# Kernel optimization log

Hardware: AMD Instinct MI355X
Metric: run time of the kernel (lower is better)

Reference implementation:

```python
import jax, jax.numpy as jnp
import numpy as np

D = 64          # d_model
H = 128         # ffn_hidden_dim
N = 10000       # nodes
E = 50000       # edges
NEG_SLOPE = 0.01  # LeakyReLU default


def setup_inputs() -> dict:
    key = jax.random.key(0)
    ks = jax.random.split(key, 10)
    x = jax.random.normal(ks[0], (N, D), dtype=jnp.float32)
    edge_index = jax.random.randint(ks[1], (2, E), 0, N)
    edge_attr = jax.random.normal(ks[2], (E, D), dtype=jnp.float32)
    # MapE2NxN params (stored as [in, out] so forward is x @ W + b)
    w1 = jax.random.normal(ks[3], (D, H), dtype=jnp.float32) / np.sqrt(D)
    b1 = jnp.zeros((H,), dtype=jnp.float32)
    w2 = jax.random.normal(ks[4], (H, D * D), dtype=jnp.float32) / np.sqrt(H)
    b2 = jnp.zeros((D * D,), dtype=jnp.float32)
    # NNConv root weight + bias
    root = jax.random.normal(ks[5], (D, D), dtype=jnp.float32) / np.sqrt(D)
    bias = jnp.zeros((D,), dtype=jnp.float32)
    # LayerNorm affine params
    gamma = jnp.ones((D,), dtype=jnp.float32)
    beta = jnp.zeros((D,), dtype=jnp.float32)
    return {"x": x, "edge_attr": edge_attr, "gamma": gamma, "beta": beta,
            "w1": w1, "b1": b1, "w2": w2, "b2": b2,
            "root": root, "bias": bias, "edge_index": edge_index}


def _layer_norm(h, gamma, beta, eps=1e-5):
    mu = jnp.mean(h, axis=-1, keepdims=True)
    var = jnp.var(h, axis=-1, keepdims=True)
    return (h - mu) * jax.lax.rsqrt(var + eps) * gamma + beta


def _leaky_relu(h):
    return jnp.where(h >= 0, h, NEG_SLOPE * h)


def reference(x, edge_attr, gamma, beta, w1, b1, w2, b2, root, bias, edge_index):
    src, dst = edge_index[0], edge_index[1]
    # DeepGCNLayer block='res+': pre-activation norm -> act -> (dropout p=0) -> conv -> residual
    h = _leaky_relu(_layer_norm(x, gamma, beta))
    # MapE2NxN on edge attributes -> per-edge [D, D] weight matrix
    we = _leaky_relu(edge_attr @ w1 + b1) @ w2 + b2   # [E, D*D]
    we = we.reshape(E, D, D)
    # per-edge matvec with source node features (PyG NNConv message)
    msg = jnp.einsum('ed,edf->ef', h[src], we)        # [E, D]
    # scatter-mean aggregate into destination nodes
    agg = jax.ops.segment_sum(msg, dst, num_segments=N)
    cnt = jax.ops.segment_sum(jnp.ones((E,), dtype=msg.dtype), dst, num_segments=N)
    agg = agg / jnp.maximum(cnt, 1.0)[:, None]
    # root transform + bias, then residual
    out = agg + h @ root + bias
    return x + out
```

## Files before the change

### kernel.cpp

```cpp
#include <hip/hip_runtime.h>

#define NS 10000
#define DD 64
#define HH 128
#define EE 50000
#define SLOPE 0.01f

typedef __attribute__((ext_vector_type(8))) short short8;
typedef __attribute__((ext_vector_type(4))) float f32x4;

static __device__ __forceinline__ unsigned short f2bf(float f) {
  unsigned int u = __float_as_uint(f);
  u += 0x7fff + ((u >> 16) & 1);
  return (unsigned short)(u >> 16);
}

__device__ __forceinline__ float wave_sum64(float v) {
  #pragma unroll
  for (int m = 32; m >= 1; m >>= 1) v += __shfl_xor(v, m, 64);
  return v;
}

__global__ __launch_bounds__(256) void k_prep(const float* __restrict__ x,
    const float* __restrict__ gamma, const float* __restrict__ beta,
    float* __restrict__ h, unsigned short* __restrict__ hbf,
    const float* __restrict__ ea, unsigned short* __restrict__ eabf,
    const float* __restrict__ w2, unsigned short* __restrict__ w2t2,
    const float* __restrict__ w1, unsigned short* __restrict__ w1t,
    const float* __restrict__ b2, unsigned short* __restrict__ b2t,
    const int* __restrict__ ei, int* __restrict__ cntsrc,
    int* __restrict__ cntdst) {
  int gid = blockIdx.x * 256 + threadIdx.x;
  if (gid < EE) {
    atomicAdd(&cntsrc[ei[gid]], 1);
    atomicAdd(&cntdst[ei[EE + gid]], 1);
  }
  if (gid < EE * DD / 8) {
    const float4* sp = (const float4*)(ea + (size_t)gid * 8);
    float4 v0 = sp[0], v1 = sp[1];
    short8 o;
    o[0] = f2bf(v0.x); o[1] = f2bf(v0.y); o[2] = f2bf(v0.z); o[3] = f2bf(v0.w);
    o[4] = f2bf(v1.x); o[5] = f2bf(v1.y); o[6] = f2bf(v1.z); o[7] = f2bf(v1.w);
    *(short8*)(eabf + (size_t)gid * 8) = o;
  }
  if (gid < HH * DD * DD) {
    int d = gid & 63;
    int c2 = gid >> 6;
    int f = c2 >> 7, k = c2 & 127;
    w2t2[gid] = f2bf(w2[k * (DD * DD) + d * DD + f]);
  }
  if (gid < DD * HH) {
    int d = gid & 63, hc = gid >> 6;
    w1t[gid] = f2bf(w1[d * HH + hc]);
  }
  if (gid < DD * DD) {
    int d = gid & 63, f = gid >> 6;
    b2t[gid] = f2bf(b2[d * DD + f]);
  }
  int wid = threadIdx.x >> 6;
  int lane = threadIdx.x & 63;
  int row = blockIdx.x * 4 + wid;
  if (row >= NS) return;
  float v = x[row * DD + lane];
  float s = wave_sum64(v);
  float s2 = wave_sum64(v * v);
  float mu = s * (1.0f / 64.0f);
  float var = s2 * (1.0f / 64.0f) - mu * mu;
  float r = rsqrtf(var + 1e-5f);
  float hn = (v - mu) * r * gamma[lane] + beta[lane];
  float hv = hn >= 0.f ? hn : SLOPE * hn;
  h[row * DD + lane] = hv;
  hbf[row * DD + lane] = f2bf(hv);
}

__global__ __launch_bounds__(1024) void k_scan(const int* __restrict__ cntsrc,
    int* __restrict__ rowptr, int* __restrict__ cursor) {
  __shared__ int ps[1024];
  int t = threadIdx.x;
  const int CH = (NS + 1023) / 1024;
  int base = t * CH;
  int sum = 0;
  for (int i = 0; i < CH; ++i) {
    int idx = base + i;
    if (idx < NS) sum += cntsrc[idx];
  }
  ps[t] = sum;
  __syncthreads();
  for (int off = 1; off < 1024; off <<= 1) {
    int v = (t >= off) ? ps[t - off] : 0;
    __syncthreads();
    ps[t] += v;
    __syncthreads();
  }
  int run = ps[t] - sum;
  for (int i = 0; i < CH; ++i) {
    int idx = base + i;
    if (idx < NS) {
      rowptr[idx] = run;
      cursor[idx] = run;
      run += cntsrc[idx];
    }
  }
  if (t == 1023) rowptr[NS] = run;
}

#define UBLK 782
#define CBLK 157
__global__ __launch_bounds__(256) void k_mid(
    const unsigned short* __restrict__ eabf, const unsigned short* __restrict__ w1t,
    const float* __restrict__ b1, unsigned short* __restrict__ ubf,
    const unsigned short* __restrict__ hbf, const unsigned short* __restrict__ b2t,
    float* __restrict__ cc, const int* __restrict__ ei,
    int* __restrict__ cursor, int* __restrict__ eord) {
  int t = threadIdx.x;
  int bid = blockIdx.x;
  int gid = bid * 256 + t;
  if (gid < EE) {
    int s = ei[gid];
    int pos = atomicAdd(&cursor[s], 1);
    eord[pos] = gid;
  }
  int w = t >> 6, lane = t & 63, lr = lane & 15, lg = lane >> 4;
  if (bid < UBLK) {
    int r0 = bid * 64 + w * 16;
    int ra = r0 + lr; if (ra >= EE) ra = EE - 1;
    short8 a0 = *(const short8*)(eabf + (size_t)ra * DD + lg * 8);
    short8 a1 = *(const short8*)(eabf + (size_t)ra * DD + 32 + lg * 8);
    short8 bb0[8], bb1[8];
    #pragma unroll
    for (int ni = 0; ni < 8; ++ni) {
      const unsigned short* bp = w1t + (ni * 16 + lr) * DD;
      bb0[ni] = *(const short8*)(bp + lg * 8);
      bb1[ni] = *(const short8*)(bp + 32 + lg * 8);
    }
    f32x4 acc[8] = {};
    #pragma unroll
    for (int ni = 0; ni < 8; ++ni) {
      acc[ni] = __builtin_amdgcn_mfma_f32_16x16x32_bf16(a0, bb0[ni], acc[ni], 0, 0, 0);
      acc[ni] = __builtin_amdgcn_mfma_f32_16x16x32_bf16(a1, bb1[ni], acc[ni], 0, 0, 0);
    }
    #pragma unroll
    for (int ni = 0; ni < 8; ++ni) {
      int col = ni * 16 + lr;
      float bb = b1[col];
      #pragma unroll
      for (int reg = 0; reg < 4; ++reg) {
        int gr = r0 + lg * 4 + reg;
        if (gr < EE) {
          float vv = acc[ni][reg] + bb;
          ubf[(size_t)gr * HH + col] = f2bf(vv >= 0.f ? vv : SLOPE * vv);
        }
      }
    }
  } else if (bid < UBLK + CBLK) {
    int row0 = (bid - UBLK) * 64;
    short8 a[4][2];
    #pragma unroll
    for (int mi = 0; mi < 4; ++mi) {
      int ra = row0 + mi * 16 + lr; if (ra >= NS) ra = NS - 1;
      a[mi][0] = *(const short8*)(hbf + (size_t)ra * DD + lg * 8);
      a[mi][1] = *(const short8*)(hbf + (size_t)ra * DD + 32 + lg * 8);
    }
    const unsigned short* bp = b2t + (w * 16 + lr) * DD;
    short8 b0 = *(const short8*)(bp + lg * 8);
    short8 b1v = *(const short8*)(bp + 32 + lg * 8);
    f32x4 acc[4] = {};
    #pragma unroll
    for (int mi = 0; mi < 4; ++mi) {
      acc[mi] = __builtin_amdgcn_mfma_f32_16x16x32_bf16(a[mi][0], b0, acc[mi], 0, 0, 0);
      acc[mi] = __builtin_amdgcn_mfma_f32_16x16x32_bf16(a[mi][1], b1v, acc[mi], 0, 0, 0);
    }
    #pragma unroll
    for (int mi = 0; mi < 4; ++mi)
      #pragma unroll
      for (int reg = 0; reg < 4; ++reg) {
        int gr = row0 + mi * 16 + lg * 4 + reg;
        if (gr < NS) cc[(size_t)gr * DD + w * 16 + lr] = acc[mi][reg];
      }
  }
}

__global__ __launch_bounds__(256) void k_T_mfma(
    const unsigned short* __restrict__ hbf, const unsigned short* __restrict__ w2t2,
    unsigned short* __restrict__ T, int n0, int n1) {
  __shared__ unsigned short As[64][72];
  __shared__ unsigned short Bs[256 * 72];
  int t = threadIdx.x;
  int row0 = n0 + blockIdx.x * 64;
  int col0 = blockIdx.y * 256;
  #pragma unroll
  for (int i = 0; i < 2; ++i) {
    int idx = t + i * 256;
    int r = idx >> 3, cc = (idx & 7) * 8;
    int gr = row0 + r;
    short8 v = {};
    if (gr < n1) v = *(const short8*)(hbf + (size_t)gr * DD + cc);
    *(short8*)(&As[r][cc]) = v;
  }
  #pragma unroll
  for (int i = 0; i < 8; ++i) {
    int idx = t + i * 256;
    int cL = idx >> 3, rr = (idx & 7) * 8;
    int gc = col0 + cL;
    short8 v = *(const short8*)(w2t2 + (size_t)gc * DD + rr);
    *(short8*)(&Bs[cL * 72 + rr]) = v;
  }
  __syncthreads();
  int w = t >> 6, lane = t & 63;
  int lr = lane & 15, lg = lane >> 4;
  f32x4 acc[4][4] = {};
  #pragma unroll
  for (int kk = 0; kk < 64; kk += 32) {
    short8 a[4], b[4];
    #pragma unroll
    for (int mi = 0; mi < 4; ++mi)
      a[mi] = *(const short8*)(&As[mi * 16 + lr][kk + lg * 8]);
    #pragma unroll
    for (int ni = 0; ni < 4; ++ni)
      b[ni] = *(const short8*)(&Bs[(w * 64 + ni * 16 + lr) * 72 + kk + lg * 8]);
    #pragma unroll
    for (int mi = 0; mi < 4; ++mi)
      #pragma unroll
      for (int ni = 0; ni < 4; ++ni)
        acc[mi][ni] = __builtin_amdgcn_mfma_f32_16x16x32_bf16(
            a[mi], b[ni], acc[mi][ni], 0, 0, 0);
  }
  __syncthreads();
  #pragma unroll
  for (int mi = 0; mi < 4; ++mi)
    #pragma unroll
    for (int ni = 0; ni < 4; ++ni) {
      int col = w * 64 + ni * 16 + lr;
      #pragma unroll
      for (int reg = 0; reg < 4; ++reg)
        Bs[(mi * 16 + lg * 4 + reg) * 268 + col] = f2bf(acc[mi][ni][reg]);
    }
  __syncthreads();
  #pragma unroll
  for (int i = 0; i < 8; ++i) {
    int idx = t + i * 256;
    int row = idx >> 5, seg = idx & 31;
    int gr = row0 + row;
    if (gr < n1) {
      short8 v = *(const short8*)(&Bs[row * 268 + seg * 8]);
      *(short8*)(T + (size_t)(gr - n0) * (HH * DD) + col0 + seg * 8) = v;
    }
  }
}

__global__ __launch_bounds__(256) void k_msg_wave(
    const unsigned short* __restrict__ ubf, const unsigned short* __restrict__ T,
    const float* __restrict__ cc, const int* __restrict__ ei,
    const int* __restrict__ rowptr, const int* __restrict__ eord,
    float* __restrict__ agg, int n0, int n1) {
  int wid = threadIdx.x >> 6;
  int lane = threadIdx.x & 63;
  int s = n0 + blockIdx.x * 4 + wid;
  if (s >= n1) return;
  int beg = rowptr[s];
  int deg = rowptr[s + 1] - beg;
  if (deg == 0) return;
  int lr = lane & 15, lg = lane >> 4;
  int ev = 0, dv = 0;
  if (lane < 16 && lane < deg) {
    ev = eord[beg + lane];
    dv = ei[EE + ev];
  }
  const unsigned short* tp = T + (size_t)(s - n0) * (HH * DD);
  short8 b[4][4];
  #pragma unroll
  for (int ft = 0; ft < 4; ++ft)
    #pragma unroll
    for (int kk = 0; kk < 4; ++kk)
      b[ft][kk] =
          *(const short8*)(tp + (ft * 16 + lr) * HH + kk * 32 + lg * 8);
  float clv[4];
  #pragma unroll
  for (int ft = 0; ft < 4; ++ft) clv[ft] = cc[(size_t)s * DD + ft * 16 + lr];

  for (int p0 = 0; p0 < deg; p0 += 16) {
    if (p0) {
      ev = 0; dv = 0;
      if (lane < 16 && p0 + lane < deg) {
        ev = eord[beg + p0 + lane];
        dv = ei[EE + ev];
      }
    }
    int el = __shfl(ev, (p0 + lr < deg) ? lr : 0);
    const unsigned short* up = ubf + (size_t)el * HH;
    short8 au[4];
    #pragma unroll
    for (int kk = 0; kk < 4; ++kk)
      au[kk] = *(const short8*)(up + kk * 32 + lg * 8);
    f32x4 acc[4] = {};
    #pragma unroll
    for (int kk = 0; kk < 4; ++kk)
      #pragma unroll
      for (int ft = 0; ft < 4; ++ft)
        acc[ft] = __builtin_amdgcn_mfma_f32_16x16x32_bf16(au[kk], b[ft][kk],
                                                          acc[ft], 0, 0, 0);
    #pragma unroll
    for (int reg = 0; reg < 4; ++reg) {
      int eidx = p0 + lg * 4 + reg;
      int dstn = __shfl(dv, lg * 4 + reg);
      if (eidx < deg) {
        #pragma unroll
        for (int ft = 0; ft < 4; ++ft)
          atomicAdd(&agg[(size_t)dstn * DD + ft * 16 + lr],
                    acc[ft][reg] + clv[ft]);
      }
    }
  }
}

__global__ __launch_bounds__(256) void k_final(const float* __restrict__ x,
    const float* __restrict__ h, const float* __restrict__ root,
    const float* __restrict__ bias, const float* __restrict__ agg,
    const int* __restrict__ cnt, float* __restrict__ out) {
  __shared__ float Bs[DD][DD + 1];
  __shared__ float As[32][DD];
  int t = threadIdx.x;
  #pragma unroll
  for (int i = 0; i < 16; ++i) {
    int idx = t + i * 256;
    Bs[idx >> 6][idx & 63] = root[idx];
  }
  int row0 = blockIdx.x * 32;
  #pragma unroll
  for (int i = 0; i < 8; ++i) {
    int idx = t + i * 256;
    int r = idx >> 6, d = idx & 63;
    int gr = row0 + r;
    As[r][d] = (gr < NS) ? h[gr * DD + d] : 0.f;
  }
  __syncthreads();
  int r = t >> 3;
  int c0 = (t & 7) * 8;
  int gr = row0 + r;
  if (gr >= NS) return;
  float acc[8] = {};
  for (int d = 0; d < DD; ++d) {
    float a = As[r][d];
    #pragma unroll
    for (int j = 0; j < 8; ++j) acc[j] += a * Bs[d][c0 + j];
  }
  float inv = 1.0f / fmaxf((float)cnt[gr], 1.0f);
  #pragma unroll
  for (int j = 0; j < 8; ++j) {
    size_t gi = (size_t)gr * DD + c0 + j;
    out[gi] = x[gi] + agg[gi] * inv + acc[j] + bias[c0 + j];
  }
}

extern "C" void kernel_launch(void* const* d_in, const int* in_sizes, int n_in,
                              void* d_out, int out_size, void* d_ws, size_t ws_size,
                              hipStream_t stream) {
  const float* x     = (const float*)d_in[0];
  const float* ea    = (const float*)d_in[1];
  const float* gamma = (const float*)d_in[2];
  const float* beta  = (const float*)d_in[3];
  const float* w1    = (const float*)d_in[4];
  const float* b1    = (const float*)d_in[5];
  const float* w2    = (const float*)d_in[6];
  const float* b2    = (const float*)d_in[7];
  const float* root  = (const float*)d_in[8];
  const float* bias  = (const float*)d_in[9];
  const int*   ei    = (const int*)d_in[10];
  float* out = (float*)d_out;

  char* p = (char*)d_ws;
  auto carve = [&](size_t bytes) {
    char* q = p;
    p += (bytes + 255) & ~(size_t)255;
    return q;
  };
  float* h             = (float*)carve(sizeof(float) * NS * DD);
  unsigned short* hbf  = (unsigned short*)carve(sizeof(short) * NS * DD);
  float* cc            = (float*)carve(sizeof(float) * NS * DD);
  unsigned short* w2t2 = (unsigned short*)carve(sizeof(short) * HH * DD * DD);
  unsigned short* w1t  = (unsigned short*)carve(sizeof(short) * DD * HH);
  unsigned short* b2t  = (unsigned short*)carve(sizeof(short) * DD * DD);
  unsigned short* eabf = (unsigned short*)carve(sizeof(short) * (size_t)EE * DD);
  unsigned short* ubf  = (unsigned short*)carve(sizeof(short) * (size_t)EE * HH);
  int* rowptr          = (int*)carve(sizeof(int) * (NS + 1));
  int* cursor          = (int*)carve(sizeof(int) * NS);
  int* eord            = (int*)carve(sizeof(int) * EE);
  char* z0 = p;
  float* agg           = (float*)carve(sizeof(float) * NS * DD);
  int* cntdst          = (int*)carve(sizeof(int) * NS);
  int* cntsrc          = (int*)carve(sizeof(int) * NS);
  size_t zlen = (size_t)(p - z0);
  size_t fixed = (size_t)(p - (char*)d_ws);

  size_t freeb = (ws_size > fixed) ? (ws_size - fixed - 256) : 0;
  int rows = (int)(freeb / (sizeof(short) * HH * DD));
  if (rows > NS) rows = NS;
  rows &= ~63;
  if (rows < 64) rows = 64;
  unsigned short* Tt = (unsigned short*)carve(sizeof(short) * (size_t)rows * HH * DD);

  hipMemsetAsync(z0, 0, zlen, stream);

  k_prep<<<dim3((NS + 3) / 4), dim3(256), 0, stream>>>(
      x, gamma, beta, h, hbf, ea, eabf, w2, w2t2, w1, w1t, b2, b2t,
      ei, cntsrc, cntdst);
  k_scan<<<dim3(1), dim3(1024), 0, stream>>>(cntsrc, rowptr, cursor);
  k_mid<<<dim3(UBLK + CBLK), dim3(256), 0, stream>>>(
      eabf, w1t, b1, ubf, hbf, b2t, cc, ei, cursor, eord);

  for (int n0 = 0; n0 < NS; n0 += rows) {
    int n1 = n0 + rows;
    if (n1 > NS) n1 = NS;
    int nr = n1 - n0;
    k_T_mfma<<<dim3((nr + 63) / 64, (HH * DD) / 256), dim3(256), 0, stream>>>(
        hbf, w2t2, Tt, n0, n1);
    k_msg_wave<<<dim3((nr + 3) / 4), dim3(256), 0, stream>>>(
        ubf, Tt, cc, ei, rowptr, eord, agg, n0, n1);
  }

  k_final<<<dim3((NS + 31) / 32), dim3(256), 0, stream>>>(x, h, root, bias, agg,
                                                          cntdst, out);
}
```

Baseline: 140.4 us.

## Fuse w2 transpose with zeroing kernel, pad grids and remap message blocks

Replaces the hipMemsetAsync and the strided per-element w2 transpose inside k_prep with a dedicated kernel. That kernel zeroes the accumulator region and transposes w2 through shared memory, writing coalesced bf16 vectors. k_T_mfma's grid is padded to a multiple of 8 with an early exit for the extra blocks. k_msg_wave now uses a 2D grid so each x-block covers 64 source nodes, matching T's row tiling, which is likely meant to improve L2 locality. The chunk size also no longer rounds down when the whole node set fits.

New measurement: 130.2 us. -7.3%, faster.

```diff
diff --git a/kernel.cpp b/kernel.cpp
--- a/kernel.cpp
+++ b/kernel.cpp
@@ -21,11 +21,34 @@
   return v;
 }
 
+__global__ __launch_bounds__(256) void k_tw2z(const float* __restrict__ w2,
+    unsigned short* __restrict__ w2t2, float4* __restrict__ zbase, int zn4) {
+  __shared__ float tile[64][65];
+  int t = threadIdx.x;
+  int k = blockIdx.x;
+  for (int off = k * 256 + t; off < zn4; off += 128 * 256)
+    zbase[off] = make_float4(0.f, 0.f, 0.f, 0.f);
+  #pragma unroll
+  for (int i = 0; i < 16; ++i) {
+    int idx = t + i * 256;
+    tile[idx >> 6][idx & 63] = w2[k * (DD * DD) + idx];
+  }
+  __syncthreads();
+  #pragma unroll
+  for (int it = 0; it < 2; ++it) {
+    int slot = t + it * 256;
+    int f = slot >> 3, l8 = slot & 7;
+    short8 o;
+    #pragma unroll
+    for (int j = 0; j < 8; ++j) o[j] = f2bf(tile[l8 * 8 + j][f]);
+    *(short8*)(w2t2 + ((size_t)(f * HH + k)) * DD + l8 * 8) = o;
+  }
+}
+
 __global__ __launch_bounds__(256) void k_prep(const float* __restrict__ x,
     const float* __restrict__ gamma, const float* __restrict__ beta,
     float* __restrict__ h, unsigned short* __restrict__ hbf,
     const float* __restrict__ ea, unsigned short* __restrict__ eabf,
-    const float* __restrict__ w2, unsigned short* __restrict__ w2t2,
     const float* __restrict__ w1, unsigned short* __restrict__ w1t,
     const float* __restrict__ b2, unsigned short* __restrict__ b2t,
     const int* __restrict__ ei, int* __restrict__ cntsrc,
@@ -42,12 +65,6 @@
     o[0] = f2bf(v0.x); o[1] = f2bf(v0.y); o[2] = f2bf(v0.z); o[3] = f2bf(v0.w);
     o[4] = f2bf(v1.x); o[5] = f2bf(v1.y); o[6] = f2bf(v1.z); o[7] = f2bf(v1.w);
     *(short8*)(eabf + (size_t)gid * 8) = o;
-  }
-  if (gid < HH * DD * DD) {
-    int d = gid & 63;
-    int c2 = gid >> 6;
-    int f = c2 >> 7, k = c2 & 127;
-    w2t2[gid] = f2bf(w2[k * (DD * DD) + d * DD + f]);
   }
   if (gid < DD * HH) {
     int d = gid & 63, hc = gid >> 6;
@@ -187,6 +204,7 @@
   __shared__ unsigned short Bs[256 * 72];
   int t = threadIdx.x;
   int row0 = n0 + blockIdx.x * 64;
+  if (row0 >= n1) return;
   int col0 = blockIdx.y * 256;
   #pragma unroll
   for (int i = 0; i < 2; ++i) {
@@ -255,7 +273,7 @@
     float* __restrict__ agg, int n0, int n1) {
   int wid = threadIdx.x >> 6;
   int lane = threadIdx.x & 63;
-  int s = n0 + blockIdx.x * 4 + wid;
+  int s = n0 + blockIdx.x * 64 + blockIdx.y * 4 + wid;
   if (s >= n1) return;
   int beg = rowptr[s];
   int deg = rowptr[s + 1] - beg;
@@ -394,16 +412,14 @@
 
   size_t freeb = (ws_size > fixed) ? (ws_size - fixed - 256) : 0;
   int rows = (int)(freeb / (sizeof(short) * HH * DD));
-  if (rows > NS) rows = NS;
-  rows &= ~63;
-  if (rows < 64) rows = 64;
+  if (rows >= NS) rows = NS;
+  else { rows &= ~63; if (rows < 64) rows = 64; }
   unsigned short* Tt = (unsigned short*)carve(sizeof(short) * (size_t)rows * HH * DD);
 
-  hipMemsetAsync(z0, 0, zlen, stream);
-
+  k_tw2z<<<dim3(HH), dim3(256), 0, stream>>>(w2, w2t2, (float4*)z0,
+                                             (int)(zlen / 16));
   k_prep<<<dim3((NS + 3) / 4), dim3(256), 0, stream>>>(
-      x, gamma, beta, h, hbf, ea, eabf, w2, w2t2, w1, w1t, b2, b2t,
-      ei, cntsrc, cntdst);
+      x, gamma, beta, h, hbf, ea, eabf, w1, w1t, b2, b2t, ei, cntsrc, cntdst);
   k_scan<<<dim3(1), dim3(1024), 0, stream>>>(cntsrc, rowptr, cursor);
   k_mid<<<dim3(UBLK + CBLK), dim3(256), 0, stream>>>(
       eabf, w1t, b1, ubf, hbf, b2t, cc, ei, cursor, eord);
@@ -412,9 +428,10 @@
     int n1 = n0 + rows;
     if (n1 > NS) n1 = NS;
     int nr = n1 - n0;
-    k_T_mfma<<<dim3((nr + 63) / 64, (HH * DD) / 256), dim3(256), 0, stream>>>(
+    int gx = (((nr + 63) / 64) + 7) & ~7;
+    k_T_mfma<<<dim3(gx, (HH * DD) / 256), dim3(256), 0, stream>>>(
         hbf, w2t2, Tt, n0, n1);
-    k_msg_wave<<<dim3((nr + 3) / 4), dim3(256), 0, stream>>>(
+    k_msg_wave<<<dim3(gx, 16), dim3(256), 0, stream>>>(
         ubf, Tt, cc, ei, rowptr, eord, agg, n0, n1);
   }
 
```
